# Kernel optimization log

Hardware: AMD Instinct MI355X
Metric: run time of the kernel (lower is better)

## Reference

```python
import jax, jax.numpy as jnp
import numpy as np

B, P, K, KS = 512, 64, 30, 4      # graphs, nodes per graph, sort-pool k, conv1d kernel
N, E, F, H = B * P, 524288, 128, 256
N_CLASSES = 10
L_OUT = K - KS + 1                 # 27, conv1d output length


def _sage(h, wl, wr, b, src, dst, inv_deg):
    # PyG SAGEConv (mean aggr): out = lin_l(mean_j x_j) + lin_r(x_i); bias only on lin_l
    agg = jax.ops.segment_sum(h[src], dst, num_segments=N) * inv_deg
    return jax.nn.relu(agg @ wl + b + h @ wr)


def setup_inputs() -> dict:
    key = jax.random.key(0)
    ks = jax.random.split(key, 32)
    x = jax.random.normal(ks[0], (N, F), jnp.float32)
    # intra-graph random edges (src -> dst aggregation)
    g = jax.random.randint(ks[1], (E,), 0, B)
    src = g * P + jax.random.randint(ks[2], (E,), 0, P)
    dst = g * P + jax.random.randint(ks[3], (E,), 0, P)
    edge_index = jnp.stack([src, dst]).astype(jnp.int32)
    batch = jnp.repeat(jnp.arange(B), P).astype(jnp.int32)  # sorted graph ids

    def lin(k, i, o):
        return jax.random.normal(k, (i, o), jnp.float32) / np.float32(np.sqrt(i))

    inp = {"x": x, "edge_index": edge_index, "batch": batch}
    dims = [(F, H), (H, H), (H, H), (H, H)]
    ki = 4
    for li, (i, o) in enumerate(dims):
        inp[f"sage{li}_wl"] = lin(ks[ki], i, o); ki += 1
        inp[f"sage{li}_wr"] = lin(ks[ki], i, o); ki += 1
        inp[f"sage{li}_b"] = jnp.zeros((o,), jnp.float32)
    inp["conv1d_w"] = jax.random.normal(ks[ki], (H, H, KS), jnp.float32) / np.float32(np.sqrt(H * KS)); ki += 1
    inp["conv1d_b"] = jnp.zeros((H,), jnp.float32)
    inp["lin1_w"] = lin(ks[ki], H * L_OUT, H); ki += 1
    inp["lin1_b"] = jnp.zeros((H,), jnp.float32)
    inp["lin2_w"] = lin(ks[ki], H, 128); ki += 1
    inp["lin2_b"] = jnp.zeros((128,), jnp.float32)
    inp["out_w"] = lin(ks[ki], 128, N_CLASSES); ki += 1
    inp["out_b"] = jnp.zeros((N_CLASSES,), jnp.float32)
    return inp


def reference(x, edge_index, batch,
              sage0_wl, sage0_wr, sage0_b,
              sage1_wl, sage1_wr, sage1_b,
              sage2_wl, sage2_wr, sage2_b,
              sage3_wl, sage3_wr, sage3_b,
              conv1d_w, conv1d_b, lin1_w, lin1_b,
              lin2_w, lin2_b, out_w, out_b):
    src, dst = edge_index[0], edge_index[1]
    deg = jax.ops.segment_sum(jnp.ones(src.shape, x.dtype), dst, num_segments=N)
    inv_deg = (1.0 / jnp.maximum(deg, 1.0))[:, None]

    h = jnp.nan_to_num(x, nan=0.0)
    h = _sage(h, sage0_wl, sage0_wr, sage0_b, src, dst, inv_deg)
    h = _sage(h, sage1_wl, sage1_wr, sage1_b, src, dst, inv_deg)
    h = _sage(h, sage2_wl, sage2_wr, sage2_b, src, dst, inv_deg)
    h = _sage(h, sage3_wl, sage3_wr, sage3_b, src, dst, inv_deg)  # [N, H]

    # SortAggregation(k=K): to dense batch, sort by last channel desc, top-k, zero-pad
    counts = jax.ops.segment_sum(jnp.ones(N, jnp.int32), batch, num_segments=B)
    offsets = jnp.cumsum(counts) - counts
    pos = jnp.arange(N) - offsets[batch]
    D = h.shape[1]
    dense = jnp.zeros((B, P, D), h.dtype).at[batch, pos].set(h)
    valid = jnp.zeros((B, P), bool).at[batch, pos].set(True)
    skey = jnp.where(valid, dense[..., -1], -jnp.inf)
    order = jnp.argsort(-skey, axis=1)[:, :K]                       # [B, K]
    topk = jnp.take_along_axis(dense, order[..., None], axis=1)     # [B, K, D]
    tvalid = jnp.take_along_axis(valid, order, axis=1)
    topk = jnp.where(tvalid[..., None], topk, 0.0)

    # x.view(B, K, -1).permute(0, 2, 1) -> [B, D, K]
    xc = topk.transpose(0, 2, 1)
    y = jax.lax.conv_general_dilated(xc, conv1d_w, (1,), 'VALID',
                                     dimension_numbers=('NCH', 'OIH', 'NCH'))
    y = jax.nn.relu(y + conv1d_b[None, :, None])                    # [B, H, L_OUT]
    y = y.reshape(B, -1)                                            # dropout is identity in eval
    y = jax.nn.relu(y @ lin1_w + lin1_b)
    y = jax.nn.relu(y @ lin2_w + lin2_b)
    return jax.nn.relu(y @ out_w + out_b)                           # [B, N_CLASSES]
```

## Files before the change

### kernel.cpp

```cpp
#include <hip/hip_runtime.h>
#include <hip/hip_bf16.h>

#define NNODES 32768
#define NEDGES 524288
#define NGRAPH 512
#define PNODES 64
#define KTOP 30
#define FIN 128
#define HID 256
#define LOUT 27

#define C1F 4.8828125e-4f
#define C2F 2.384185791015625e-7f

using f16x8 = __attribute__((ext_vector_type(8))) _Float16;
using f16x4 = __attribute__((ext_vector_type(4))) _Float16;
using f32x4 = __attribute__((ext_vector_type(4))) float;
using f32x16 = __attribute__((ext_vector_type(16))) float;

#define GLDS(src, dst) __builtin_amdgcn_global_load_lds( \
    (const __attribute__((address_space(1))) void*)(src), \
    (__attribute__((address_space(3))) void*)(dst), 16, 0, 0)

__global__ void hist_kernel(const int* __restrict__ dst, int* __restrict__ counts) {
    int e = blockIdx.x * blockDim.x + threadIdx.x;
    if (e < NEDGES) atomicAdd(&counts[dst[e]], 1);
}

__global__ __launch_bounds__(1024) void scan_block_kernel(const int* __restrict__ counts,
        int* __restrict__ loc, int* __restrict__ partial) {
    int b = blockIdx.x, t = threadIdx.x;
    int i = b * 1024 + t;
    int v = counts[i];
    int lane = t & 63, w = t >> 6;
    int x = v;
    #pragma unroll
    for (int d = 1; d < 64; d <<= 1) { int y = __shfl_up(x, d, 64); if (lane >= d) x += y; }
    __shared__ int ws[16];
    if (lane == 63) ws[w] = x;
    __syncthreads();
    if (w == 0) {
        int s = (lane < 16) ? ws[lane] : 0;
        #pragma unroll
        for (int d = 1; d < 16; d <<= 1) { int y = __shfl_up(s, d, 64); if (lane >= d) s += y; }
        if (lane < 16) ws[lane] = s;
    }
    __syncthreads();
    int base = (w > 0) ? ws[w - 1] : 0;
    int incl = base + x;
    loc[i] = incl - v;
    if (t == 1023) partial[b] = incl;
}

__global__ __launch_bounds__(1024) void scan_fixup_kernel(const int* __restrict__ loc,
        const int* __restrict__ partial, const int* __restrict__ counts,
        int* __restrict__ offsets, int* __restrict__ cursor, float* __restrict__ invdeg) {
    int b = blockIdx.x, t = threadIdx.x;
    int i = b * 1024 + t;
    __shared__ int sbase;
    if (t == 0) { int s = 0; for (int j = 0; j < b; ++j) s += partial[j]; sbase = s; }
    __syncthreads();
    int o = loc[i] + sbase;
    offsets[i] = o;
    cursor[i] = o;
    invdeg[i] = 1.0f / fmaxf((float)counts[i], 1.0f);
}

__global__ void scatter_kernel(const int* __restrict__ src, const int* __restrict__ dst,
        int* __restrict__ cursor, int* __restrict__ ssrc) {
    int e = blockIdx.x * blockDim.x + threadIdx.x;
    if (e < NEDGES) {
        int d = dst[e];
        int p = atomicAdd(&cursor[d], 1);
        ssrc[p] = src[e];
    }
}

__global__ void nan2num_split_kernel(const float* __restrict__ x,
        _Float16* __restrict__ oh, _Float16* __restrict__ ol, int n4) {
    int i = blockIdx.x * blockDim.x + threadIdx.x;
    if (i >= n4) return;
    float4 v = *(const float4*)(x + i * 4);
    float xs[4] = {v.x, v.y, v.z, v.w};
    f16x4 hh, ll;
    #pragma unroll
    for (int q = 0; q < 4; ++q) {
        float a = xs[q];
        a = (a != a) ? 0.f : a;
        _Float16 h = (_Float16)a;
        hh[q] = h;
        ll[q] = (_Float16)((a - (float)h) * 2048.0f);
    }
    *(f16x4*)(oh + (size_t)i * 4) = hh;
    *(f16x4*)(ol + (size_t)i * 4) = ll;
}

struct Prep8 {
    const float* src[8];
    _Float16* dh[8];
    _Float16* dl[8];
    int logK[8];
    int nelem[8];
};

__global__ __launch_bounds__(256) void prep8_kernel(Prep8 p) {
    int y = blockIdx.y;
    int idx = blockIdx.x * 256 + threadIdx.x;
    if (idx >= p.nelem[y]) return;
    int lk = p.logK[y], K = 1 << lk;
    int n = idx >> lk, k = idx & (K - 1);
    float w = p.src[y][(size_t)k * 256 + n];
    _Float16 h = (_Float16)w;
    p.dh[y][(size_t)n * K + k] = h;
    p.dl[y][(size_t)n * K + k] = (_Float16)((w - (float)h) * 2048.0f);
}

__global__ __launch_bounds__(256) void prep_conv_kernel(const float* __restrict__ W,
        _Float16* __restrict__ b0, _Float16* __restrict__ b1) {
    int idx = blockIdx.x * 256 + threadIdx.x;
    int o = idx >> 10, k = idx & 1023;
    float w = W[(size_t)o * 1024 + (k & 255) * 4 + (k >> 8)];
    _Float16 h = (_Float16)w;
    b0[(size_t)o * 1024 + k] = h;
    b1[(size_t)o * 1024 + k] = (_Float16)((w - (float)h) * 2048.0f);
}

__global__ __launch_bounds__(256) void prep_lin1_kernel(const float* __restrict__ l1w,
        _Float16* __restrict__ wh, _Float16* __restrict__ wl_) {
    __shared__ float sh[64][65];
    int kb = blockIdx.x * 64;
    int nb = blockIdx.y * 64;
    int t = threadIdx.x;
    {
        int kk = t >> 2;
        int nc = (t & 3) * 16;
        int k = kb + kk, l = k >> 8, c = k & 255;
        const float* srow = l1w + (size_t)(c * 27 + l) * 256 + nb + nc;
        #pragma unroll
        for (int j = 0; j < 16; j += 4) {
            float4 v = *(const float4*)(srow + j);
            sh[kk][nc + j + 0] = v.x;
            sh[kk][nc + j + 1] = v.y;
            sh[kk][nc + j + 2] = v.z;
            sh[kk][nc + j + 3] = v.w;
        }
    }
    __syncthreads();
    {
        int nn = t >> 2;
        int kc = (t & 3) * 16;
        f16x8 oh[2], ol[2];
        #pragma unroll
        for (int j = 0; j < 16; ++j) {
            float x = sh[kc + j][nn];
            _Float16 h = (_Float16)x;
            oh[j >> 3][j & 7] = h;
            ol[j >> 3][j & 7] = (_Float16)((x - (float)h) * 2048.0f);
        }
        size_t o = (size_t)(nb + nn) * 6912 + kb + kc;
        *(f16x8*)(wh + o) = oh[0];
        *(f16x8*)(wh + o + 8) = oh[1];
        *(f16x8*)(wl_ + o) = ol[0];
        *(f16x8*)(wl_ + o + 8) = ol[1];
    }
}

template<int H, int LOGH>
__global__ __launch_bounds__(256) void aggregate_ps_kernel(
        const _Float16* __restrict__ hh, const _Float16* __restrict__ hl,
        const int* __restrict__ offsets, const int* __restrict__ counts,
        const int* __restrict__ ssrc, const float* __restrict__ invdeg,
        _Float16* __restrict__ aggh, _Float16* __restrict__ aggl) {
    __shared__ float sh[64 * H];
    const int g = blockIdx.x, t = threadIdx.x;
    const size_t base = (size_t)g * 64 * H;
    for (int i4 = t * 4; i4 < 64 * H; i4 += 1024) {
        f16x4 vh = *(const f16x4*)(hh + base + i4);
        f16x4 vl = *(const f16x4*)(hl + base + i4);
        int row = i4 >> LOGH, col = i4 & (H - 1);
        int sw = row & 28;
        float4 v = make_float4(
            (float)vh[0] + C1F * (float)vl[0],
            (float)vh[1] + C1F * (float)vl[1],
            (float)vh[2] + C1F * (float)vl[2],
            (float)vh[3] + C1F * (float)vl[3]);
        *(float4*)&sh[(row << LOGH) + (col ^ sw)] = v;
    }
    __syncthreads();
    const int n = t >> 2, fb = t & 3;
    const int FQ = H >> 2;
    const int node = g * 64 + n;
    const int beg = offsets[node], cnt = counts[node];
    float acc[FQ];
    #pragma unroll
    for (int j = 0; j < FQ; ++j) acc[j] = 0.f;
    for (int e = 0; e < cnt; ++e) {
        int sn = ssrc[beg + e] & 63;
        int rowoff = sn << LOGH;
        int sw = sn & 28;
        #pragma unroll
        for (int j = 0; j < FQ; j += 4) {
            int f = fb * FQ + (j ^ (fb * 8));
            float4 v = *(float4*)&sh[rowoff + (f ^ sw)];
            acc[j]     += v.x;
            acc[j + 1] += v.y;
            acc[j + 2] += v.z;
            acc[j + 3] += v.w;
        }
    }
    float s = invdeg[node];
    __syncthreads();
    {
        int rowoff = n << LOGH;
        int sw = n & 28;
        #pragma unroll
        for (int j = 0; j < FQ; j += 4) {
            int f = fb * FQ + (j ^ (fb * 8));
            *(float4*)&sh[rowoff + (f ^ sw)] =
                make_float4(acc[j] * s, acc[j + 1] * s, acc[j + 2] * s, acc[j + 3] * s);
        }
    }
    __syncthreads();
    for (int i4 = t * 4; i4 < 64 * H; i4 += 1024) {
        int row = i4 >> LOGH, col = i4 & (H - 1);
        int sw = row & 28;
        float4 v = *(float4*)&sh[(row << LOGH) + (col ^ sw)];
        float xs[4] = {v.x, v.y, v.z, v.w};
        f16x4 oh, ol;
        #pragma unroll
        for (int q = 0; q < 4; ++q) {
            _Float16 h = (_Float16)xs[q];
            oh[q] = h;
            ol[q] = (_Float16)((xs[q] - (float)h) * 2048.0f);
        }
        *(f16x4*)(aggh + base + i4) = oh;
        *(f16x4*)(aggl + base + i4) = ol;
    }
}

template<int NPROD, int CONV, int NPAIRS, int EPI>
__global__ __launch_bounds__(256, 2) void mfma_ps_kernel(
        const _Float16* __restrict__ A1h, const _Float16* __restrict__ A1l,
        const _Float16* __restrict__ A2h, const _Float16* __restrict__ A2l,
        const _Float16* __restrict__ B1h, const _Float16* __restrict__ B1l,
        const _Float16* __restrict__ B2h, const _Float16* __restrict__ B2l,
        const float* __restrict__ bias,
        _Float16* __restrict__ outh, _Float16* __restrict__ outl,
        float* __restrict__ Cpart,
        int lda, int K, int Nd, int nrb) {
    __shared__ _Float16 As[2][2][128 * 32];
    __shared__ _Float16 Bs[2][2][128 * 32];
    const int t = threadIdx.x;
    const int lane = t & 63, wave = t >> 6;
    const int wr = wave & 1, wc = wave >> 1;
    const int bid = blockIdx.x;
    const int rb = bid % nrb, cb = bid / nrb;
    const int row0 = rb * 128, col0 = cb * 128;
    const int l31 = lane & 31, hb = lane >> 5, x3 = l31 & 3;
    const int r16 = lane >> 2;
    const int qsrc8 = ((lane & 3) ^ (r16 & 3)) * 8;
    size_t aoffj[2], boffj[2];
    #pragma unroll
    for (int j = 0; j < 2; ++j) {
        int ar = row0 + wave * 32 + j * 16 + r16;
        aoffj[j] = CONV ? ((size_t)ar * 256 + (size_t)(ar / 27) * 768)
                        : (size_t)ar * (size_t)lda;
        boffj[j] = (size_t)(col0 + wave * 32 + j * 16 + r16) * (size_t)K;
    }
    int aroff[2], broff[2], slot8[2];
    #pragma unroll
    for (int mi = 0; mi < 2; ++mi) aroff[mi] = (wr * 64 + mi * 32 + l31) * 32;
    #pragma unroll
    for (int ni = 0; ni < 2; ++ni) broff[ni] = (wc * 64 + ni * 32 + l31) * 32;
    #pragma unroll
    for (int h = 0; h < 2; ++h) slot8[h] = ((2 * h + hb) ^ x3) * 8;

    const int KV = NPAIRS * K;
    const int kchunk = KV / gridDim.z;
    const int kv_lo = blockIdx.z * kchunk, kv_hi = kv_lo + kchunk;

    f32x16 acc0[2][2], acc1[2][2], acc2[2][2];
    #pragma unroll
    for (int i = 0; i < 2; ++i)
        #pragma unroll
        for (int j = 0; j < 2; ++j) { acc0[i][j] = 0.f; acc1[i][j] = 0.f; acc2[i][j] = 0.f; }

    auto stage = [&](int kv, int b) {
        int p = (NPAIRS == 2 && kv >= K) ? 1 : 0;
        int k = kv - p * K;
        const _Float16* __restrict__ sAh = p ? A2h : A1h;
        const _Float16* __restrict__ sAl = p ? A2l : A1l;
        const _Float16* __restrict__ sBh = p ? B2h : B1h;
        const _Float16* __restrict__ sBl = p ? B2l : B1l;
        #pragma unroll
        for (int j = 0; j < 2; ++j) {
            int ldsbase = (wave * 32 + j * 16) * 32;
            size_t ga = aoffj[j] + k + qsrc8;
            size_t gb = boffj[j] + k + qsrc8;
            GLDS(sAh + ga, &As[b][0][ldsbase]);
            GLDS(sAl + ga, &As[b][1][ldsbase]);
            GLDS(sBh + gb, &Bs[b][0][ldsbase]);
            GLDS(sBl + gb, &Bs[b][1][ldsbase]);
        }
    };

    stage(kv_lo, 0);
    __syncthreads();
    int b = 0;
    for (int kv = kv_lo; kv < kv_hi; kv += 32) {
        if (kv + 32 < kv_hi) stage(kv + 32, b ^ 1);
        #pragma unroll
        for (int h = 0; h < 2; ++h) {
            f16x8 af0[2], af1[2], bf0[2], bf1[2];
            #pragma unroll
            for (int mi = 0; mi < 2; ++mi) {
                af0[mi] = *(const f16x8*)&As[b][0][aroff[mi] + slot8[h]];
                af1[mi] = *(const f16x8*)&As[b][1][aroff[mi] + slot8[h]];
            }
            #pragma unroll
            for (int ni = 0; ni < 2; ++ni) {
                bf0[ni] = *(const f16x8*)&Bs[b][0][broff[ni] + slot8[h]];
                bf1[ni] = *(const f16x8*)&Bs[b][1][broff[ni] + slot8[h]];
            }
            #pragma unroll
            for (int mi = 0; mi < 2; ++mi)
                #pragma unroll
                for (int ni = 0; ni < 2; ++ni) {
                    acc0[mi][ni] = __builtin_amdgcn_mfma_f32_32x32x16_f16(af0[mi], bf0[ni], acc0[mi][ni], 0, 0, 0);
                    acc1[mi][ni] = __builtin_amdgcn_mfma_f32_32x32x16_f16(af1[mi], bf0[ni], acc1[mi][ni], 0, 0, 0);
                    acc1[mi][ni] = __builtin_amdgcn_mfma_f32_32x32x16_f16(af0[mi], bf1[ni], acc1[mi][ni], 0, 0, 0);
                    if (NPROD == 4)
                        acc2[mi][ni] = __builtin_amdgcn_mfma_f32_32x32x16_f16(af1[mi], bf1[ni], acc2[mi][ni], 0, 0, 0);
                }
        }
        b ^= 1;
        __syncthreads();
    }

    const int rquad = 4 * hb;
    #pragma unroll
    for (int ni = 0; ni < 2; ++ni) {
        int col = col0 + wc * 64 + ni * 32 + l31;
        float bb = (EPI == 0) ? bias[col] : 0.f;
        #pragma unroll
        for (int mi = 0; mi < 2; ++mi) {
            #pragma unroll
            for (int reg = 0; reg < 16; ++reg) {
                float v = acc0[mi][ni][reg] + C1F * acc1[mi][ni][reg];
                if (NPROD == 4) v += C2F * acc2[mi][ni][reg];
                int row = row0 + wr * 64 + mi * 32 + (reg & 3) + 8 * (reg >> 2) + rquad;
                if (EPI == 0) {
                    v = fmaxf(v + bb, 0.f);
                    _Float16 h = (_Float16)v;
                    size_t o = (size_t)row * Nd + col;
                    outh[o] = h;
                    outl[o] = (_Float16)((v - (float)h) * 2048.0f);
                } else {
                    size_t zb = (size_t)blockIdx.z * (size_t)(nrb * 128) * Nd;
                    Cpart[zb + (size_t)row * Nd + col] = v;
                }
            }
        }
    }
}

__global__ __launch_bounds__(256) void sortgather_kernel(const _Float16* __restrict__ hh,
        const _Float16* __restrict__ hl, _Float16* __restrict__ th, _Float16* __restrict__ tl) {
    __shared__ float vals[PNODES];
    __shared__ int ord[KTOP];
    int g = blockIdx.x, t = threadIdx.x;
    if (t < PNODES) {
        size_t idx = (size_t)(g * PNODES + t) * HID + (HID - 1);
        vals[t] = (float)hh[idx] + C1F * (float)hl[idx];
    }
    __syncthreads();
    if (t < PNODES) {
        float v = vals[t];
        int rank = 0;
        for (int j = 0; j < PNODES; ++j) {
            float vj = vals[j];
            rank += (vj > v) || (vj == v && j < t);
        }
        if (rank < KTOP) ord[rank] = g * PNODES + t;
    }
    __syncthreads();
    for (int r = 0; r < KTOP; ++r) {
        size_t s = (size_t)ord[r] * HID + t;
        size_t d = (size_t)(g * KTOP + r) * HID + t;
        th[d] = hh[s];
        tl[d] = hl[s];
    }
}

__global__ void reduce_conv_kernel(const float* __restrict__ yb32,
        const float* __restrict__ b, _Float16* __restrict__ ybh, _Float16* __restrict__ ybl) {
    int i = blockIdx.x * 256 + threadIdx.x;
    float v = fmaxf(yb32[i] + yb32[i + 13824 * 256] + b[i & 255], 0.f);
    _Float16 h = (_Float16)v;
    ybh[i] = h;
    ybl[i] = (_Float16)((v - (float)h) * 2048.0f);
}

__global__ void reduce_lin1_kernel(const float* __restrict__ z1p,
        const float* __restrict__ b, float* __restrict__ z1) {
    int i = blockIdx.x * 256 + threadIdx.x;
    float s = b[i & 255];
    #pragma unroll
    for (int z = 0; z < 27; ++z) s += z1p[(size_t)z * 131072 + i];
    z1[i] = fmaxf(s, 0.f);
}

__global__ __launch_bounds__(256) void gemm64_kernel(
        const float* __restrict__ A, const float* __restrict__ B,
        const float* __restrict__ bias, float* __restrict__ C,
        int lda, int kend, int Nd) {
    __shared__ float As[16][64];
    __shared__ float Bs[16][64];
    const int tid = threadIdx.x;
    const int tx = tid & 15, ty = tid >> 4;
    const int la_r = tid >> 2, la_c = (tid & 3) << 2;
    const int lb_r = tid >> 4, lb_c = (tid & 15) << 2;
    const int row0 = blockIdx.x * 64, col0 = blockIdx.y * 64;
    const size_t aoff = (size_t)(row0 + la_r) * (size_t)lda;
    float acc[4][4] = {};
    for (int k0 = 0; k0 < kend; k0 += 16) {
        __syncthreads();
        float4 av = *(const float4*)(A + aoff + k0 + la_c);
        As[la_c + 0][la_r] = av.x;
        As[la_c + 1][la_r] = av.y;
        As[la_c + 2][la_r] = av.z;
        As[la_c + 3][la_r] = av.w;
        *(float4*)&Bs[lb_r][lb_c] = *(const float4*)(B + (size_t)(k0 + lb_r) * Nd + col0 + lb_c);
        __syncthreads();
        #pragma unroll
        for (int k = 0; k < 16; ++k) {
            float4 a = *(const float4*)&As[k][ty << 2];
            float4 b = *(const float4*)&Bs[k][tx << 2];
            acc[0][0] += a.x * b.x; acc[0][1] += a.x * b.y; acc[0][2] += a.x * b.z; acc[0][3] += a.x * b.w;
            acc[1][0] += a.y * b.x; acc[1][1] += a.y * b.y; acc[1][2] += a.y * b.z; acc[1][3] += a.y * b.w;
            acc[2][0] += a.z * b.x; acc[2][1] += a.z * b.y; acc[2][2] += a.z * b.z; acc[2][3] += a.z * b.w;
            acc[3][0] += a.w * b.x; acc[3][1] += a.w * b.y; acc[3][2] += a.w * b.z; acc[3][3] += a.w * b.w;
        }
    }
    #pragma unroll
    for (int i = 0; i < 4; ++i) {
        int row = row0 + (ty << 2) + i;
        #pragma unroll
        for (int j = 0; j < 4; ++j) {
            int col = col0 + (tx << 2) + j;
            C[(size_t)row * Nd + col] = fmaxf(acc[i][j] + bias[col], 0.f);
        }
    }
}

__global__ void out_kernel(const float* __restrict__ z2, const float* __restrict__ w,
        const float* __restrict__ b, float* __restrict__ out) {
    int idx = blockIdx.x * blockDim.x + threadIdx.x;
    if (idx < NGRAPH * 10) {
        int r = idx / 10, c = idx % 10;
        float s = b[c];
        for (int k = 0; k < 128; ++k) s += z2[r * 128 + k] * w[k * 10 + c];
        out[idx] = fmaxf(s, 0.f);
    }
}

extern "C" void kernel_launch(void* const* d_in, const int* in_sizes, int n_in,
                              void* d_out, int out_size, void* d_ws, size_t ws_size,
                              hipStream_t stream) {
    const float* x    = (const float*)d_in[0];
    const int*   edge = (const int*)d_in[1];
    const int*   esrc = edge;
    const int*   edst = edge + NEDGES;
    const float* wl[4] = {(const float*)d_in[3], (const float*)d_in[6], (const float*)d_in[9],  (const float*)d_in[12]};
    const float* wr[4] = {(const float*)d_in[4], (const float*)d_in[7], (const float*)d_in[10], (const float*)d_in[13]};
    const float* sb[4] = {(const float*)d_in[5], (const float*)d_in[8], (const float*)d_in[11], (const float*)d_in[14]};
    const float* convw = (const float*)d_in[15];
    const float* convb = (const float*)d_in[16];
    const float* l1w   = (const float*)d_in[17];
    const float* l1b   = (const float*)d_in[18];
    const float* l2w   = (const float*)d_in[19];
    const float* l2b   = (const float*)d_in[20];
    const float* ow    = (const float*)d_in[21];
    const float* ob    = (const float*)d_in[22];
    float* out = (float*)d_out;

    char* ws = (char*)d_ws;
    size_t off = 0;
    auto alloc = [&](size_t bytes) -> char* {
        char* p = ws + off;
        off = (off + bytes + 255) & ~(size_t)255;
        return p;
    };
    int*   counts  = (int*)alloc((size_t)NNODES * 4);
    int*   offsets = (int*)alloc((size_t)NNODES * 4);
    int*   cursor  = (int*)alloc((size_t)NNODES * 4);
    int*   loc     = (int*)alloc((size_t)NNODES * 4);
    int*   partial = (int*)alloc(32 * 4);
    float* invdeg  = (float*)alloc((size_t)NNODES * 4);
    int*   ssrc    = (int*)alloc((size_t)NEDGES * 4);
    _Float16* wlh[4]; _Float16* wll[4]; _Float16* wrh[4]; _Float16* wrl[4];
    for (int l = 0; l < 4; ++l) {
        size_t kb = (size_t)(l ? HID : FIN) * HID * 2;
        wlh[l] = (_Float16*)alloc(kb); wll[l] = (_Float16*)alloc(kb);
        wrh[l] = (_Float16*)alloc(kb); wrl[l] = (_Float16*)alloc(kb);
    }
    _Float16* cvh = (_Float16*)alloc((size_t)HID * 1024 * 2);
    _Float16* cvl = (_Float16*)alloc((size_t)HID * 1024 * 2);

    const size_t H0T = (size_t)NNODES * FIN * 2;
    const size_t AGT = (size_t)NNODES * HID * 2;
    const size_t TKT = (size_t)NGRAPH * KTOP * HID * 2;
    const size_t YBT = (size_t)NGRAPH * LOUT * HID * 2;
    const size_t YB32T = (size_t)2 * 13824 * 256 * 4;
    const size_t Z1PT = (size_t)27 * NGRAPH * HID * 4;
    const size_t W1T = (size_t)HID * 6912 * 2;

    char* R1 = alloc(2 * H0T);
    char* R2 = alloc(2 * AGT);
    char* R3 = alloc(2 * AGT);
    char* R4 = alloc(2 * AGT);
    _Float16* h0h = (_Float16*)R1; _Float16* h0l = (_Float16*)(R1 + H0T);
    _Float16* tkh = (_Float16*)R1; _Float16* tkl = (_Float16*)(R1 + TKT);
    _Float16* aggh = (_Float16*)R2; _Float16* aggl = (_Float16*)(R2 + AGT);
    _Float16* hAh = (_Float16*)R3; _Float16* hAl = (_Float16*)(R3 + AGT);
    _Float16* ybh = (_Float16*)R2; _Float16* ybl_ = (_Float16*)(R2 + YBT);
    float* yb32 = (float*)(R2 + 2 * YBT);
    float* z1p  = (float*)(R2 + 2 * YBT);
    char* tail2 = R2 + 2 * YBT + YB32T;
    float* z1  = (float*)tail2;
    float* z2  = (float*)(tail2 + (size_t)NGRAPH * HID * 4);
    _Float16* w1h = (_Float16*)(tail2 + (size_t)NGRAPH * HID * 4 + (size_t)NGRAPH * 128 * 4 + 256);
    _Float16* w1l = (_Float16*)((char*)w1h + W1T);
    _Float16* hBh = (_Float16*)R4; _Float16* hBl = (_Float16*)(R4 + AGT);

    hipMemsetAsync(counts, 0, (size_t)NNODES * 4, stream);
    hist_kernel<<<NEDGES / 256, 256, 0, stream>>>(edst, counts);
    scan_block_kernel<<<NNODES / 1024, 1024, 0, stream>>>(counts, loc, partial);
    scan_fixup_kernel<<<NNODES / 1024, 1024, 0, stream>>>(loc, partial, counts, offsets, cursor, invdeg);
    scatter_kernel<<<NEDGES / 256, 256, 0, stream>>>(esrc, edst, cursor, ssrc);
    nan2num_split_kernel<<<(NNODES * FIN / 4) / 256, 256, 0, stream>>>(x, h0h, h0l, NNODES * FIN / 4);

    Prep8 p8;
    for (int l = 0; l < 4; ++l) {
        int K = l ? HID : FIN, lk = l ? 8 : 7;
        p8.src[2 * l] = wl[l];     p8.dh[2 * l] = wlh[l];     p8.dl[2 * l] = wll[l];
        p8.src[2 * l + 1] = wr[l]; p8.dh[2 * l + 1] = wrh[l]; p8.dl[2 * l + 1] = wrl[l];
        p8.logK[2 * l] = lk;   p8.nelem[2 * l] = 256 * K;
        p8.logK[2 * l + 1] = lk; p8.nelem[2 * l + 1] = 256 * K;
    }
    prep8_kernel<<<dim3(256, 8), 256, 0, stream>>>(p8);
    prep_conv_kernel<<<(HID * 1024) / 256, 256, 0, stream>>>(convw, cvh, cvl);

    aggregate_ps_kernel<FIN, 7><<<NGRAPH, 256, 0, stream>>>(h0h, h0l, offsets, counts, ssrc, invdeg, aggh, aggl);
    mfma_ps_kernel<3, 0, 2, 0><<<dim3(256 * 2, 1, 1), 256, 0, stream>>>(
        aggh, aggl, h0h, h0l, wlh[0], wll[0], wrh[0], wrl[0], sb[0], hAh, hAl, nullptr, FIN, FIN, HID, 256);
    _Float16* hinh = hAh; _Float16* hinl = hAl;
    _Float16* hoth = hBh; _Float16* hotl = hBl;
    for (int l = 1; l < 4; ++l) {
        aggregate_ps_kernel<HID, 8><<<NGRAPH, 256, 0, stream>>>(hinh, hinl, offsets, counts, ssrc, invdeg, aggh, aggl);
        mfma_ps_kernel<3, 0, 2, 0><<<dim3(256 * 2, 1, 1), 256, 0, stream>>>(
            aggh, aggl, hinh, hinl, wlh[l], wll[l], wrh[l], wrl[l], sb[l], hoth, hotl, nullptr, HID, HID, HID, 256);
        _Float16* t1 = hinh; hinh = hoth; hoth = t1;
        _Float16* t2 = hinl; hinl = hotl; hotl = t2;
    }

    sortgather_kernel<<<NGRAPH, 256, 0, stream>>>(hinh, hinl, tkh, tkl);
    prep_lin1_kernel<<<dim3(108, 4), 256, 0, stream>>>(l1w, w1h, w1l);

    mfma_ps_kernel<3, 1, 1, 1><<<dim3(108 * 2, 1, 2), 256, 0, stream>>>(
        tkh, tkl, nullptr, nullptr, cvh, cvl, nullptr, nullptr, nullptr, nullptr, nullptr, yb32, 256, 1024, HID, 108);
    reduce_conv_kernel<<<13824 * 256 / 256, 256, 0, stream>>>(yb32, convb, ybh, ybl_);

    mfma_ps_kernel<3, 0, 1, 1><<<dim3(4 * 2, 1, 27), 256, 0, stream>>>(
        ybh, ybl_, nullptr, nullptr, w1h, w1l, nullptr, nullptr, nullptr, nullptr, nullptr, z1p, 6912, 6912, HID, 4);
    reduce_lin1_kernel<<<NGRAPH * HID / 256, 256, 0, stream>>>(z1p, l1b, z1);

    gemm64_kernel<<<dim3(NGRAPH / 64, 128 / 64), 256, 0, stream>>>(z1, l2w, l2b, z2, HID, HID, 128);

    out_kernel<<<(NGRAPH * 10 + 255) / 256, 256, 0, stream>>>(z2, ow, ob, out);
}
```

Before: 495.4 us.

## Fuse neighbor aggregation into SAGE GEMM epilogue and nan2num conversion

Removes the standalone aggregate kernels. The first layer's mean aggregation is folded into the nan2num conversion kernel. For later layers, each SAGE GEMM block writes its fp32 output tile (128 rows, i.e. two graphs × 128 columns) into LDS and computes the next layer's neighbor mean from there, writing agg hi/lo directly. This saves a full re-read of the hidden features from global memory per layer and three kernel launches. The cost is an extra LDS-heavy epilogue with 64 accumulators per thread, which adds register pressure. It also relies on edges staying within the 128-row tile, which holds because graphs are 64-node aligned.

```diff
diff --git a/kernel.cpp b/kernel.cpp
--- a/kernel.cpp
+++ b/kernel.cpp
@@ -76,23 +76,66 @@
     }
 }
 
-__global__ void nan2num_split_kernel(const float* __restrict__ x,
-        _Float16* __restrict__ oh, _Float16* __restrict__ ol, int n4) {
-    int i = blockIdx.x * blockDim.x + threadIdx.x;
-    if (i >= n4) return;
-    float4 v = *(const float4*)(x + i * 4);
-    float xs[4] = {v.x, v.y, v.z, v.w};
-    f16x4 hh, ll;
-    #pragma unroll
-    for (int q = 0; q < 4; ++q) {
-        float a = xs[q];
-        a = (a != a) ? 0.f : a;
-        _Float16 h = (_Float16)a;
-        hh[q] = h;
-        ll[q] = (_Float16)((a - (float)h) * 2048.0f);
-    }
-    *(f16x4*)(oh + (size_t)i * 4) = hh;
-    *(f16x4*)(ol + (size_t)i * 4) = ll;
+__global__ __launch_bounds__(256) void nan2num_agg_kernel(const float* __restrict__ x,
+        const int* __restrict__ offsets, const int* __restrict__ counts,
+        const int* __restrict__ ssrc, const float* __restrict__ invdeg,
+        _Float16* __restrict__ h0h, _Float16* __restrict__ h0l,
+        _Float16* __restrict__ aggh, _Float16* __restrict__ aggl) {
+    __shared__ float sh[64 * 128];
+    const int g = blockIdx.x, t = threadIdx.x;
+    const size_t base = (size_t)g * 64 * 128;
+    for (int i4 = t * 4; i4 < 64 * 128; i4 += 1024) {
+        float4 v = *(const float4*)(x + base + i4);
+        float xs[4] = {v.x, v.y, v.z, v.w};
+        f16x4 oh, ol;
+        #pragma unroll
+        for (int q = 0; q < 4; ++q) {
+            float a = xs[q];
+            a = (a != a) ? 0.f : a;
+            xs[q] = a;
+            _Float16 h = (_Float16)a;
+            oh[q] = h;
+            ol[q] = (_Float16)((a - (float)h) * 2048.0f);
+        }
+        *(f16x4*)(h0h + base + i4) = oh;
+        *(f16x4*)(h0l + base + i4) = ol;
+        int row = i4 >> 7, col = i4 & 127;
+        int sw = row & 28;
+        *(float4*)&sh[(row << 7) + (col ^ sw)] = make_float4(xs[0], xs[1], xs[2], xs[3]);
+    }
+    __syncthreads();
+    const int n = t >> 2, fb = t & 3;
+    const int node = g * 64 + n;
+    const int beg = offsets[node], cnt = counts[node];
+    float acc[32];
+    #pragma unroll
+    for (int j = 0; j < 32; ++j) acc[j] = 0.f;
+    for (int e = 0; e < cnt; ++e) {
+        int sn = ssrc[beg + e] & 63;
+        int rowoff = sn << 7;
+        int sw = sn & 28;
+        #pragma unroll
+        for (int j = 0; j < 32; j += 4) {
+            int f = fb * 32 + (j ^ (fb * 8));
+            float4 v = *(float4*)&sh[rowoff + (f ^ sw)];
+            acc[j] += v.x; acc[j + 1] += v.y; acc[j + 2] += v.z; acc[j + 3] += v.w;
+        }
+    }
+    float s = invdeg[node];
+    #pragma unroll
+    for (int j = 0; j < 32; j += 4) {
+        int f = fb * 32 + (j ^ (fb * 8));
+        f16x4 oh, ol;
+        #pragma unroll
+        for (int q = 0; q < 4; ++q) {
+            float a = acc[j + q] * s;
+            _Float16 h = (_Float16)a;
+            oh[q] = h;
+            ol[q] = (_Float16)((a - (float)h) * 2048.0f);
+        }
+        *(f16x4*)(aggh + (size_t)node * 128 + f) = oh;
+        *(f16x4*)(aggl + (size_t)node * 128 + f) = ol;
+    }
 }
 
 struct Prep8 {
@@ -165,80 +208,7 @@
     }
 }
 
-template<int H, int LOGH>
-__global__ __launch_bounds__(256) void aggregate_ps_kernel(
-        const _Float16* __restrict__ hh, const _Float16* __restrict__ hl,
-        const int* __restrict__ offsets, const int* __restrict__ counts,
-        const int* __restrict__ ssrc, const float* __restrict__ invdeg,
-        _Float16* __restrict__ aggh, _Float16* __restrict__ aggl) {
-    __shared__ float sh[64 * H];
-    const int g = blockIdx.x, t = threadIdx.x;
-    const size_t base = (size_t)g * 64 * H;
-    for (int i4 = t * 4; i4 < 64 * H; i4 += 1024) {
-        f16x4 vh = *(const f16x4*)(hh + base + i4);
-        f16x4 vl = *(const f16x4*)(hl + base + i4);
-        int row = i4 >> LOGH, col = i4 & (H - 1);
-        int sw = row & 28;
-        float4 v = make_float4(
-            (float)vh[0] + C1F * (float)vl[0],
-            (float)vh[1] + C1F * (float)vl[1],
-            (float)vh[2] + C1F * (float)vl[2],
-            (float)vh[3] + C1F * (float)vl[3]);
-        *(float4*)&sh[(row << LOGH) + (col ^ sw)] = v;
-    }
-    __syncthreads();
-    const int n = t >> 2, fb = t & 3;
-    const int FQ = H >> 2;
-    const int node = g * 64 + n;
-    const int beg = offsets[node], cnt = counts[node];
-    float acc[FQ];
-    #pragma unroll
-    for (int j = 0; j < FQ; ++j) acc[j] = 0.f;
-    for (int e = 0; e < cnt; ++e) {
-        int sn = ssrc[beg + e] & 63;
-        int rowoff = sn << LOGH;
-        int sw = sn & 28;
-        #pragma unroll
-        for (int j = 0; j < FQ; j += 4) {
-            int f = fb * FQ + (j ^ (fb * 8));
-            float4 v = *(float4*)&sh[rowoff + (f ^ sw)];
-            acc[j]     += v.x;
-            acc[j + 1] += v.y;
-            acc[j + 2] += v.z;
-            acc[j + 3] += v.w;
-        }
-    }
-    float s = invdeg[node];
-    __syncthreads();
-    {
-        int rowoff = n << LOGH;
-        int sw = n & 28;
-        #pragma unroll
-        for (int j = 0; j < FQ; j += 4) {
-            int f = fb * FQ + (j ^ (fb * 8));
-            *(float4*)&sh[rowoff + (f ^ sw)] =
-                make_float4(acc[j] * s, acc[j + 1] * s, acc[j + 2] * s, acc[j + 3] * s);
-        }
-    }
-    __syncthreads();
-    for (int i4 = t * 4; i4 < 64 * H; i4 += 1024) {
-        int row = i4 >> LOGH, col = i4 & (H - 1);
-        int sw = row & 28;
-        float4 v = *(float4*)&sh[(row << LOGH) + (col ^ sw)];
-        float xs[4] = {v.x, v.y, v.z, v.w};
-        f16x4 oh, ol;
-        #pragma unroll
-        for (int q = 0; q < 4; ++q) {
-            _Float16 h = (_Float16)xs[q];
-            oh[q] = h;
-            ol[q] = (_Float16)((xs[q] - (float)h) * 2048.0f);
-        }
-        *(f16x4*)(aggh + base + i4) = oh;
-        *(f16x4*)(aggl + base + i4) = ol;
-    }
-}
-
-template<int NPROD, int CONV, int NPAIRS, int EPI>
+template<int NPROD, int CONV, int NPAIRS, int EPI, int AGG>
 __global__ __launch_bounds__(256, 2) void mfma_ps_kernel(
         const _Float16* __restrict__ A1h, const _Float16* __restrict__ A1l,
         const _Float16* __restrict__ A2h, const _Float16* __restrict__ A2l,
@@ -247,9 +217,14 @@
         const float* __restrict__ bias,
         _Float16* __restrict__ outh, _Float16* __restrict__ outl,
         float* __restrict__ Cpart,
+        _Float16* __restrict__ aggoh, _Float16* __restrict__ aggol,
+        const int* __restrict__ offsets, const int* __restrict__ counts,
+        const int* __restrict__ ssrc, const float* __restrict__ invdeg,
         int lda, int K, int Nd, int nrb) {
-    __shared__ _Float16 As[2][2][128 * 32];
-    __shared__ _Float16 Bs[2][2][128 * 32];
+    __shared__ _Float16 smem[32768];
+    _Float16* const As0 = smem;
+    _Float16* const Bs0 = smem + 16384;
+    float* const tile = (float*)smem;
     const int t = threadIdx.x;
     const int lane = t & 63, wave = t >> 6;
     const int wr = wave & 1, wc = wave >> 1;
@@ -297,10 +272,10 @@
             int ldsbase = (wave * 32 + j * 16) * 32;
             size_t ga = aoffj[j] + k + qsrc8;
             size_t gb = boffj[j] + k + qsrc8;
-            GLDS(sAh + ga, &As[b][0][ldsbase]);
-            GLDS(sAl + ga, &As[b][1][ldsbase]);
-            GLDS(sBh + gb, &Bs[b][0][ldsbase]);
-            GLDS(sBl + gb, &Bs[b][1][ldsbase]);
+            GLDS(sAh + ga, As0 + b * 8192 + ldsbase);
+            GLDS(sAl + ga, As0 + b * 8192 + 4096 + ldsbase);
+            GLDS(sBh + gb, Bs0 + b * 8192 + ldsbase);
+            GLDS(sBl + gb, Bs0 + b * 8192 + 4096 + ldsbase);
         }
     };
 
@@ -314,13 +289,13 @@
             f16x8 af0[2], af1[2], bf0[2], bf1[2];
             #pragma unroll
             for (int mi = 0; mi < 2; ++mi) {
-                af0[mi] = *(const f16x8*)&As[b][0][aroff[mi] + slot8[h]];
-                af1[mi] = *(const f16x8*)&As[b][1][aroff[mi] + slot8[h]];
+                af0[mi] = *(const f16x8*)(As0 + b * 8192 + aroff[mi] + slot8[h]);
+                af1[mi] = *(const f16x8*)(As0 + b * 8192 + 4096 + aroff[mi] + slot8[h]);
             }
             #pragma unroll
             for (int ni = 0; ni < 2; ++ni) {
-                bf0[ni] = *(const f16x8*)&Bs[b][0][broff[ni] + slot8[h]];
-                bf1[ni] = *(const f16x8*)&Bs[b][1][broff[ni] + slot8[h]];
+                bf0[ni] = *(const f16x8*)(Bs0 + b * 8192 + broff[ni] + slot8[h]);
+                bf1[ni] = *(const f16x8*)(Bs0 + b * 8192 + 4096 + broff[ni] + slot8[h]);
             }
             #pragma unroll
             for (int mi = 0; mi < 2; ++mi)
@@ -340,7 +315,8 @@
     const int rquad = 4 * hb;
     #pragma unroll
     for (int ni = 0; ni < 2; ++ni) {
-        int col = col0 + wc * 64 + ni * 32 + l31;
+        int tc = wc * 64 + ni * 32 + l31;
+        int col = col0 + tc;
         float bb = (EPI == 0) ? bias[col] : 0.f;
         #pragma unroll
         for (int mi = 0; mi < 2; ++mi) {
@@ -348,18 +324,55 @@
             for (int reg = 0; reg < 16; ++reg) {
                 float v = acc0[mi][ni][reg] + C1F * acc1[mi][ni][reg];
                 if (NPROD == 4) v += C2F * acc2[mi][ni][reg];
-                int row = row0 + wr * 64 + mi * 32 + (reg & 3) + 8 * (reg >> 2) + rquad;
+                int tr = wr * 64 + mi * 32 + (reg & 3) + 8 * (reg >> 2) + rquad;
+                int row = row0 + tr;
                 if (EPI == 0) {
                     v = fmaxf(v + bb, 0.f);
                     _Float16 h = (_Float16)v;
                     size_t o = (size_t)row * Nd + col;
                     outh[o] = h;
                     outl[o] = (_Float16)((v - (float)h) * 2048.0f);
+                    if (AGG) tile[tr * 128 + (tc ^ (tr & 28))] = v;
                 } else {
                     size_t zb = (size_t)blockIdx.z * (size_t)(nrb * 128) * Nd;
                     Cpart[zb + (size_t)row * Nd + col] = v;
                 }
             }
+        }
+    }
+    if (AGG) {
+        __syncthreads();
+        const int nloc = t >> 1, fb = t & 1;
+        const int gn = row0 + nloc;
+        const int beg = offsets[gn], cnt = counts[gn];
+        float acc[64];
+        #pragma unroll
+        for (int j = 0; j < 64; ++j) acc[j] = 0.f;
+        for (int e = 0; e < cnt; ++e) {
+            int tr = ssrc[beg + e] - row0;
+            int rowoff = tr * 128, sw = tr & 28;
+            #pragma unroll
+            for (int j = 0; j < 64; j += 4) {
+                int f = fb * 64 + (j ^ (fb * 8));
+                float4 v = *(float4*)&tile[rowoff + (f ^ sw)];
+                acc[j] += v.x; acc[j + 1] += v.y; acc[j + 2] += v.z; acc[j + 3] += v.w;
+            }
+        }
+        float s = invdeg[gn];
+        #pragma unroll
+        for (int j = 0; j < 64; j += 4) {
+            int f = fb * 64 + (j ^ (fb * 8));
+            f16x4 oh, ol;
+            #pragma unroll
+            for (int q = 0; q < 4; ++q) {
+                float a = acc[j + q] * s;
+                _Float16 h = (_Float16)a;
+                oh[q] = h;
+                ol[q] = (_Float16)((a - (float)h) * 2048.0f);
+            }
+            size_t o = (size_t)gn * Nd + col0 + f;
+            *(f16x4*)(aggoh + o) = oh;
+            *(f16x4*)(aggol + o) = ol;
         }
     }
 }
@@ -512,17 +525,19 @@
     const size_t TKT = (size_t)NGRAPH * KTOP * HID * 2;
     const size_t YBT = (size_t)NGRAPH * LOUT * HID * 2;
     const size_t YB32T = (size_t)2 * 13824 * 256 * 4;
-    const size_t Z1PT = (size_t)27 * NGRAPH * HID * 4;
     const size_t W1T = (size_t)HID * 6912 * 2;
 
     char* R1 = alloc(2 * H0T);
     char* R2 = alloc(2 * AGT);
     char* R3 = alloc(2 * AGT);
     char* R4 = alloc(2 * AGT);
+    char* R5 = alloc(2 * AGT);
     _Float16* h0h = (_Float16*)R1; _Float16* h0l = (_Float16*)(R1 + H0T);
     _Float16* tkh = (_Float16*)R1; _Float16* tkl = (_Float16*)(R1 + TKT);
-    _Float16* aggh = (_Float16*)R2; _Float16* aggl = (_Float16*)(R2 + AGT);
+    _Float16* aggAh = (_Float16*)R2; _Float16* aggAl = (_Float16*)(R2 + AGT);
     _Float16* hAh = (_Float16*)R3; _Float16* hAl = (_Float16*)(R3 + AGT);
+    _Float16* hBh = (_Float16*)R4; _Float16* hBl = (_Float16*)(R4 + AGT);
+    _Float16* aggBh = (_Float16*)R5; _Float16* aggBl = (_Float16*)(R5 + AGT);
     _Float16* ybh = (_Float16*)R2; _Float16* ybl_ = (_Float16*)(R2 + YBT);
     float* yb32 = (float*)(R2 + 2 * YBT);
     float* z1p  = (float*)(R2 + 2 * YBT);
@@ -531,14 +546,14 @@
     float* z2  = (float*)(tail2 + (size_t)NGRAPH * HID * 4);
     _Float16* w1h = (_Float16*)(tail2 + (size_t)NGRAPH * HID * 4 + (size_t)NGRAPH * 128 * 4 + 256);
     _Float16* w1l = (_Float16*)((char*)w1h + W1T);
-    _Float16* hBh = (_Float16*)R4; _Float16* hBl = (_Float16*)(R4 + AGT);
 
     hipMemsetAsync(counts, 0, (size_t)NNODES * 4, stream);
     hist_kernel<<<NEDGES / 256, 256, 0, stream>>>(edst, counts);
     scan_block_kernel<<<NNODES / 1024, 1024, 0, stream>>>(counts, loc, partial);
     scan_fixup_kernel<<<NNODES / 1024, 1024, 0, stream>>>(loc, partial, counts, offsets, cursor, invdeg);
     scatter_kernel<<<NEDGES / 256, 256, 0, stream>>>(esrc, edst, cursor, ssrc);
-    nan2num_split_kernel<<<(NNODES * FIN / 4) / 256, 256, 0, stream>>>(x, h0h, h0l, NNODES * FIN / 4);
+    nan2num_agg_kernel<<<NGRAPH, 256, 0, stream>>>(x, offsets, counts, ssrc, invdeg,
+                                                   h0h, h0l, aggAh, aggAl);
 
     Prep8 p8;
     for (int l = 0; l < 4; ++l) {
@@ -551,28 +566,32 @@
     prep8_kernel<<<dim3(256, 8), 256, 0, stream>>>(p8);
     prep_conv_kernel<<<(HID * 1024) / 256, 256, 0, stream>>>(convw, cvh, cvl);
 
-    aggregate_ps_kernel<FIN, 7><<<NGRAPH, 256, 0, stream>>>(h0h, h0l, offsets, counts, ssrc, invdeg, aggh, aggl);
-    mfma_ps_kernel<3, 0, 2, 0><<<dim3(256 * 2, 1, 1), 256, 0, stream>>>(
-        aggh, aggl, h0h, h0l, wlh[0], wll[0], wrh[0], wrl[0], sb[0], hAh, hAl, nullptr, FIN, FIN, HID, 256);
-    _Float16* hinh = hAh; _Float16* hinl = hAl;
-    _Float16* hoth = hBh; _Float16* hotl = hBl;
-    for (int l = 1; l < 4; ++l) {
-        aggregate_ps_kernel<HID, 8><<<NGRAPH, 256, 0, stream>>>(hinh, hinl, offsets, counts, ssrc, invdeg, aggh, aggl);
-        mfma_ps_kernel<3, 0, 2, 0><<<dim3(256 * 2, 1, 1), 256, 0, stream>>>(
-            aggh, aggl, hinh, hinl, wlh[l], wll[l], wrh[l], wrl[l], sb[l], hoth, hotl, nullptr, HID, HID, HID, 256);
-        _Float16* t1 = hinh; hinh = hoth; hoth = t1;
-        _Float16* t2 = hinl; hinl = hotl; hotl = t2;
-    }
-
-    sortgather_kernel<<<NGRAPH, 256, 0, stream>>>(hinh, hinl, tkh, tkl);
+    mfma_ps_kernel<3, 0, 2, 0, 1><<<dim3(256 * 2, 1, 1), 256, 0, stream>>>(
+        aggAh, aggAl, h0h, h0l, wlh[0], wll[0], wrh[0], wrl[0], sb[0],
+        hAh, hAl, nullptr, aggBh, aggBl, offsets, counts, ssrc, invdeg, FIN, FIN, HID, 256);
+    mfma_ps_kernel<3, 0, 2, 0, 1><<<dim3(256 * 2, 1, 1), 256, 0, stream>>>(
+        aggBh, aggBl, hAh, hAl, wlh[1], wll[1], wrh[1], wrl[1], sb[1],
+        hBh, hBl, nullptr, aggAh, aggAl, offsets, counts, ssrc, invdeg, HID, HID, HID, 256);
+    mfma_ps_kernel<3, 0, 2, 0, 1><<<dim3(256 * 2, 1, 1), 256, 0, stream>>>(
+        aggAh, aggAl, hBh, hBl, wlh[2], wll[2], wrh[2], wrl[2], sb[2],
+        hAh, hAl, nullptr, aggBh, aggBl, offsets, counts, ssrc, invdeg, HID, HID, HID, 256);
+    mfma_ps_kernel<3, 0, 2, 0, 0><<<dim3(256 * 2, 1, 1), 256, 0, stream>>>(
+        aggBh, aggBl, hAh, hAl, wlh[3], wll[3], wrh[3], wrl[3], sb[3],
+        hBh, hBl, nullptr, nullptr, nullptr, offsets, counts, ssrc, invdeg, HID, HID, HID, 256);
+
+    sortgather_kernel<<<NGRAPH, 256, 0, stream>>>(hBh, hBl, tkh, tkl);
     prep_lin1_kernel<<<dim3(108, 4), 256, 0, stream>>>(l1w, w1h, w1l);
 
-    mfma_ps_kernel<3, 1, 1, 1><<<dim3(108 * 2, 1, 2), 256, 0, stream>>>(
-        tkh, tkl, nullptr, nullptr, cvh, cvl, nullptr, nullptr, nullptr, nullptr, nullptr, yb32, 256, 1024, HID, 108);
+    mfma_ps_kernel<3, 1, 1, 1, 0><<<dim3(108 * 2, 1, 2), 256, 0, stream>>>(
+        tkh, tkl, nullptr, nullptr, cvh, cvl, nullptr, nullptr, nullptr,
+        nullptr, nullptr, yb32, nullptr, nullptr, nullptr, nullptr, nullptr, nullptr,
+        256, 1024, HID, 108);
     reduce_conv_kernel<<<13824 * 256 / 256, 256, 0, stream>>>(yb32, convb, ybh, ybl_);
 
-    mfma_ps_kernel<3, 0, 1, 1><<<dim3(4 * 2, 1, 27), 256, 0, stream>>>(
-        ybh, ybl_, nullptr, nullptr, w1h, w1l, nullptr, nullptr, nullptr, nullptr, nullptr, z1p, 6912, 6912, HID, 4);
+    mfma_ps_kernel<3, 0, 1, 1, 0><<<dim3(4 * 2, 1, 27), 256, 0, stream>>>(
+        ybh, ybl_, nullptr, nullptr, w1h, w1l, nullptr, nullptr, nullptr,
+        nullptr, nullptr, z1p, nullptr, nullptr, nullptr, nullptr, nullptr, nullptr,
+        6912, 6912, HID, 4);
     reduce_lin1_kernel<<<NGRAPH * HID / 256, 256, 0, stream>>>(z1p, l1b, z1);
 
     gemm64_kernel<<<dim3(NGRAPH / 64, 128 / 64), 256, 0, stream>>>(z1, l2w, l2b, z2, HID, HID, 128);
```

Result: no change. 495.7 us (+0.1%).
